# Optimization experiments

Measured on AMD Instinct MI355X. Metric: run time of the kernel, lower is better.

Reference implementation:

```python
import jax, jax.numpy as jnp
import numpy as np

BS, N, T, D, R = 64, 256, 32, 512, 8
DK = D // R  # 64 == key_feature_dim


def setup_inputs() -> dict:
    key = jax.random.key(0)
    ks = jax.random.split(key, 20)
    s = 0.02
    p = lambda k, shape: jax.random.normal(k, shape, jnp.float32) * s
    return {
        "v": jax.random.normal(ks[0], (BS, N, D), jnp.float32),
        "b": jax.random.normal(ks[1], (BS, N, D), jnp.float32),
        "v_mask": jnp.ones((BS, N), jnp.float32),
        "t": jax.random.normal(ks[2], (BS, T, D), jnp.float32),
        "t_mask": jnp.ones((BS, T), jnp.float32),
        "WG1_w": p(ks[3], (D, D)), "WG1_b": p(ks[4], (D,)),
        "WG2_w": p(ks[5], (D, D)), "WG2_b": p(ks[6], (D,)),
        "WK_w": p(ks[7], (D, D)), "WK_b": p(ks[8], (D,)),
        "WQ_w": p(ks[9], (D, D)), "WQ_b": p(ks[10], (D,)),
        "WV_w": p(ks[11], (D, D)), "WV_b": p(ks[12], (D,)),
        "tc_w": p(ks[13], (D, 1)), "tc_b": p(ks[14], (1,)),
        "tmap_w": p(ks[15], (D, N * N)), "tmap_b": p(ks[16], (N * N,)),
    }


def _forward(v, b, v_mask, t, t_mask,
             WG1_w, WG1_b, WG2_w, WG2_b, WK_w, WK_b, WQ_w, WQ_b, WV_w, WV_b,
             tc_w, tc_b, tmap_w, tmap_b):
    bs, num_obj, dim = v.shape
    n_rel = R
    dk = dim // n_rel  # dim_per_rel == dim_k

    def shape4(x):  # (bs, N, D) -> (bs, R, N, dk)
        return x.reshape(bs, num_obj, n_rel, dk).transpose(0, 2, 1, 3)

    # --- text summary branch ---
    t_m = t * t_mask[:, :, None]                       # (bs, T, D)
    tc = t_m @ tc_w + tc_b                             # (bs, T, 1)
    tc = jnp.where(t_mask[:, :, None] == 0, -jnp.inf, tc)
    t_sscore = jax.nn.sigmoid(tc)                      # sigmoid(-inf) = 0 for pad
    t_summary = jnp.einsum('btd,bt->bd', t_m, t_sscore[..., 0])   # (bs, D)
    tmap = jax.nn.relu(t_summary @ tmap_w + tmap_b)
    tmap = tmap.reshape(bs, 1, num_obj, num_obj)       # broadcast over relations

    # --- geometric pairwise score ---
    wg1 = shape4((b @ WG1_w + WG1_b) * v_mask[:, :, None])
    wg2 = shape4((b @ WG2_w + WG2_b) * v_mask[:, :, None])
    w_g = jax.nn.relu(jnp.einsum('brnd,brmd->brnm', wg1, wg2)) + tmap

    # --- scaled dot-product score ---
    wk = shape4(v @ WK_w + WK_b)
    wq = shape4(v @ WQ_w + WQ_b)
    scaled_dot = jnp.einsum('brnd,brmd->brnm', wk, wq) / jnp.sqrt(jnp.float32(dk))

    # --- combine, mask, softmax, weighted sum ---
    w_mn = jnp.log(jnp.maximum(w_g, 1e-6)) + scaled_dot
    w_mn = jnp.where((v_mask == 0)[:, None, None, :], -jnp.inf, w_mn)
    attn = jax.nn.softmax(w_mn, axis=-1)               # (bs, R, N, N)

    wv = shape4(v @ WV_w + WV_b)
    out = jnp.einsum('brnm,brmd->brnd', attn, wv)
    out = out.transpose(0, 2, 1, 3).reshape(bs, num_obj, dim)
    return out + v


def reference(v, b, v_mask, t, t_mask,
              WG1_w, WG1_b, WG2_w, WG2_b, WK_w, WK_b, WQ_w, WQ_b, WV_w, WV_b,
              tc_w, tc_b, tmap_w, tmap_b):
    return _forward(v, b, v_mask, t, t_mask,
                    WG1_w, WG1_b, WG2_w, WG2_b, WK_w, WK_b, WQ_w, WQ_b,
                    WV_w, WV_b, tc_w, tc_b, tmap_w, tmap_b)
```

## Files before the change

kernel.cpp:

```cpp
#include <hip/hip_runtime.h>
#include <math.h>

#define BS 64
#define NOBJ 256
#define TTOK 32
#define DIM 512
#define NREL 8
#define DKK 64
#define NN 65536

typedef __attribute__((ext_vector_type(8))) short bf16x8;
typedef __attribute__((ext_vector_type(4))) float f32x4;

__device__ __forceinline__ unsigned short f2bf(float x) {
    union { float f; unsigned int u; } c; c.f = x;
    unsigned int u = c.u;
    return (unsigned short)((u + 0x7fffu + ((u >> 16) & 1u)) >> 16);
}
__device__ __forceinline__ float bf2f(unsigned short h) {
    union { unsigned int u; float f; } c; c.u = ((unsigned int)h) << 16;
    return c.f;
}
__device__ __forceinline__ void gl2lds16(const unsigned short* g, unsigned short* l) {
    __builtin_amdgcn_global_load_lds((const __attribute__((address_space(1))) void*)g,
                                     (__attribute__((address_space(3))) void*)l, 16, 0, 0);
}

__global__ void k_text(const float* __restrict__ tt, const float* __restrict__ t_mask,
                       const float* __restrict__ tc_w, const float* __restrict__ tc_b,
                       unsigned short* __restrict__ ts_bf) {
    int b = blockIdx.x;
    int tid = threadIdx.x;
    __shared__ float red[TTOK][8];
    __shared__ float sc[TTOK];
    {
        int tok = tid >> 3, seg = tid & 7;
        const float* tp = tt + (size_t)(b * TTOK + tok) * DIM + seg * 64;
        const float* wp = tc_w + seg * 64;
        float s = 0.f;
#pragma unroll
        for (int i = 0; i < 16; ++i) {
            float4 a = *(const float4*)(tp + i * 4);
            float4 w = *(const float4*)(wp + i * 4);
            s += a.x * w.x + a.y * w.y + a.z * w.z + a.w * w.w;
        }
        red[tok][seg] = s;
    }
    __syncthreads();
    if (tid < TTOK) {
        float s = 0.f;
#pragma unroll
        for (int i = 0; i < 8; ++i) s += red[tid][i];
        float m = t_mask[b * TTOK + tid];
        float tc = m * s + tc_b[0];
        float sig = 1.f / (1.f + __expf(-tc));
        sc[tid] = (m != 0.f) ? m * sig : 0.f;
    }
    __syncthreads();
    for (int d = tid; d < DIM; d += 256) {
        float acc = 0.f;
#pragma unroll
        for (int tok = 0; tok < TTOK; ++tok)
            acc += tt[(size_t)(b * TTOK + tok) * DIM + d] * sc[tok];
        ts_bf[b * DIM + d] = f2bf(acc);
    }
}

__global__ void k_convert(const float* __restrict__ v, const float* __restrict__ b,
                          unsigned short* __restrict__ v_bf, unsigned short* __restrict__ b_bf) {
    const float* src = blockIdx.y ? b : v;
    unsigned short* dst = blockIdx.y ? b_bf : v_bf;
    size_t i = ((size_t)blockIdx.x * 256 + threadIdx.x) * 4;
    float4 a = *(const float4*)(src + i);
    ushort4 o;
    o.x = f2bf(a.x); o.y = f2bf(a.y); o.z = f2bf(a.z); o.w = f2bf(a.w);
    *(ushort4*)(dst + i) = o;
}

__global__ void k_wt(const float* __restrict__ w0, const float* __restrict__ w1,
                     const float* __restrict__ w2, const float* __restrict__ w3,
                     const float* __restrict__ w4, unsigned short* __restrict__ WT) {
    int wsel = blockIdx.z;
    const float* W = wsel == 0 ? w0 : wsel == 1 ? w1 : wsel == 2 ? w2 : wsel == 3 ? w3 : w4;
    int k0 = blockIdx.x * 64, d0 = blockIdx.y * 64;
    __shared__ float tile[64][65];
    int tid = threadIdx.x;
#pragma unroll
    for (int p = 0; p < 16; ++p) {
        int lin = p * 256 + tid;
        int kk = lin >> 6, dd = lin & 63;
        tile[kk][dd] = W[(size_t)(k0 + kk) * DIM + d0 + dd];
    }
    __syncthreads();
    unsigned short* outp = WT + (size_t)wsel * DIM * DIM;
#pragma unroll
    for (int p = 0; p < 16; ++p) {
        int lin = p * 256 + tid;
        int dd = lin >> 6, kk = lin & 63;
        outp[(size_t)(d0 + dd) * DIM + k0 + kk] = f2bf(tile[kk][dd]);
    }
}

__launch_bounds__(64)
__global__ void k_tmap(const unsigned short* __restrict__ ts_bf,
                       const float* __restrict__ tmap_w, const float* __restrict__ tmap_b,
                       unsigned short* __restrict__ tmap) {
    int col0 = blockIdx.x * 64;
    int lane = threadIdx.x;
    int q = lane >> 4, li = lane & 15;
    f32x4 acc[4][4];
#pragma unroll
    for (int rt = 0; rt < 4; ++rt)
#pragma unroll
        for (int ct = 0; ct < 4; ++ct) acc[rt][ct] = (f32x4){0.f, 0.f, 0.f, 0.f};

    for (int kt = 0; kt < 16; ++kt) {
        int k0 = kt * 32;
        bf16x8 a[4];
#pragma unroll
        for (int rt = 0; rt < 4; ++rt)
            a[rt] = *(const bf16x8*)(ts_bf + (size_t)(rt * 16 + li) * DIM + k0 + q * 8);
#pragma unroll
        for (int ct = 0; ct < 4; ++ct) {
            const float* wp = tmap_w + (size_t)(k0 + q * 8) * NN + col0 + ct * 16 + li;
            bf16x8 bb;
#pragma unroll
            for (int j = 0; j < 8; ++j)
                bb[j] = (short)f2bf(wp[(size_t)j * NN]);
#pragma unroll
            for (int rt = 0; rt < 4; ++rt)
                acc[rt][ct] = __builtin_amdgcn_mfma_f32_16x16x32_bf16(a[rt], bb, acc[rt][ct], 0, 0, 0);
        }
    }
#pragma unroll
    for (int ct = 0; ct < 4; ++ct) {
        int j = col0 + ct * 16 + li;
        float bias = tmap_b[j];
#pragma unroll
        for (int rt = 0; rt < 4; ++rt) {
#pragma unroll
            for (int i = 0; i < 4; ++i) {
                int bb = rt * 16 + q * 4 + i;
                float val = fmaxf(acc[rt][ct][i] + bias, 0.f);
                tmap[(size_t)bb * NN + j] = f2bf(val);
            }
        }
    }
}

__launch_bounds__(256)
__global__ void k_proj(const unsigned short* __restrict__ v_bf, const unsigned short* __restrict__ b_bf,
                       const unsigned short* __restrict__ WT,
                       const float* __restrict__ bias0, const float* __restrict__ bias1,
                       const float* __restrict__ bias2, const float* __restrict__ bias3,
                       const float* __restrict__ bias4, const float* __restrict__ v_mask,
                       unsigned short* __restrict__ wg1, unsigned short* __restrict__ wg2,
                       unsigned short* __restrict__ wk, unsigned short* __restrict__ wq,
                       unsigned short* __restrict__ wvT) {
    int bx = blockIdx.x;
    int by = blockIdx.y;
    int m0 = bx * 128;
    int wsel = by >> 2;
    const unsigned short* A = (wsel < 2) ? b_bf : v_bf;
    int tid = threadIdx.x;
    int w = tid >> 6, lane = tid & 63, q = lane >> 4, li = lane & 15;
    int rh = w & 1, ch = w >> 1;

    __shared__ __align__(16) unsigned short smem[128 * 136];
    unsigned short* As = smem;
    unsigned short* Bs = smem + 4096;

    f32x4 acc[4][4];
#pragma unroll
    for (int rt = 0; rt < 4; ++rt)
#pragma unroll
        for (int ct = 0; ct < 4; ++ct) acc[rt][ct] = (f32x4){0.f, 0.f, 0.f, 0.f};

    const unsigned short* WTb = WT + (size_t)by * 128 * DIM;

    int rho = lane >> 2;
    int qs = (lane & 3) ^ ((lane >> 3) & 3);
    int rA0 = w * 16 + rho, rA1 = (w + 4) * 16 + rho;
    const unsigned short* Ag0 = A + (size_t)(m0 + rA0) * DIM + qs * 8;
    const unsigned short* Ag1 = A + (size_t)(m0 + rA1) * DIM + qs * 8;
    const unsigned short* Bg0 = WTb + (size_t)rA0 * DIM + qs * 8;
    const unsigned short* Bg1 = WTb + (size_t)rA1 * DIM + qs * 8;
    unsigned short* Al0 = As + w * 512;
    unsigned short* Al1 = As + (w + 4) * 512;
    unsigned short* Bl0 = Bs + w * 512;
    unsigned short* Bl1 = Bs + (w + 4) * 512;

    int sseg = (q ^ ((li >> 1) & 3)) * 8;

    for (int ks = 0; ks < 16; ++ks) {
        int k0 = ks * 32;
        gl2lds16(Ag0 + k0, Al0);
        gl2lds16(Ag1 + k0, Al1);
        gl2lds16(Bg0 + k0, Bl0);
        gl2lds16(Bg1 + k0, Bl1);
        __syncthreads();
        bf16x8 af[4], bfr[4];
#pragma unroll
        for (int rt = 0; rt < 4; ++rt)
            af[rt] = *(const bf16x8*)(As + (rh * 64 + rt * 16 + li) * 32 + sseg);
#pragma unroll
        for (int ct = 0; ct < 4; ++ct)
            bfr[ct] = *(const bf16x8*)(Bs + (ch * 64 + ct * 16 + li) * 32 + sseg);
#pragma unroll
        for (int rt = 0; rt < 4; ++rt)
#pragma unroll
            for (int ct = 0; ct < 4; ++ct)
                acc[rt][ct] = __builtin_amdgcn_mfma_f32_16x16x32_bf16(af[rt], bfr[ct], acc[rt][ct], 0, 0, 0);
        __syncthreads();
    }

    const float* bias = wsel == 0 ? bias0 : wsel == 1 ? bias1 : wsel == 2 ? bias2 : wsel == 3 ? bias3 : bias4;
    int dblk = (by & 3) * 128;

    if (wsel < 4) {
#pragma unroll
        for (int ct = 0; ct < 4; ++ct) {
            int d = dblk + ch * 64 + ct * 16 + li;
            float bs = bias[d];
#pragma unroll
            for (int rt = 0; rt < 4; ++rt) {
#pragma unroll
                for (int i = 0; i < 4; ++i) {
                    int bn = m0 + rh * 64 + rt * 16 + q * 4 + i;
                    float val = acc[rt][ct][i] + bs;
                    if (wsel < 2) val *= v_mask[bn];
                    unsigned short h = f2bf(val);
                    if (wsel == 0)      wg1[(size_t)bn * DIM + d] = h;
                    else if (wsel == 1) wg2[(size_t)bn * DIM + d] = h;
                    else if (wsel == 2) wk[(size_t)bn * DIM + d] = h;
                    else                wq[(size_t)bn * DIM + d] = h;
                }
            }
        }
    } else {
        unsigned short (*T)[136] = (unsigned short (*)[136])smem;
#pragma unroll
        for (int ct = 0; ct < 4; ++ct) {
            int d_local = ch * 64 + ct * 16 + li;
            float bs = bias[dblk + d_local];
#pragma unroll
            for (int rt = 0; rt < 4; ++rt) {
#pragma unroll
                for (int i = 0; i < 4; ++i) {
                    int n_local = rh * 64 + rt * 16 + q * 4 + i;
                    T[d_local][n_local] = f2bf(acc[rt][ct][i] + bs);
                }
            }
        }
        __syncthreads();
        int b = m0 >> 8, nbase = m0 & 255;
        int dl = tid >> 1;
        int nh = (tid & 1) * 64;
        int d = dblk + dl;
        int rr = d >> 6, dk = d & 63;
        unsigned short* dst = wvT + ((size_t)(b * NREL + rr) * DKK + dk) * NOBJ + nbase + nh;
#pragma unroll
        for (int k = 0; k < 8; ++k)
            *(bf16x8*)(dst + k * 8) = *(const bf16x8*)(&T[dl][nh + k * 8]);
    }
}

__launch_bounds__(256)
__global__ void k_attn(const unsigned short* __restrict__ wg1, const unsigned short* __restrict__ wg2,
                       const unsigned short* __restrict__ wk, const unsigned short* __restrict__ wq,
                       const unsigned short* __restrict__ wvT,
                       const unsigned short* __restrict__ tmap, const float* __restrict__ v_mask,
                       const float* __restrict__ v, float* __restrict__ out) {
    int br = blockIdx.x;
    int b = br >> 3, r = br & 7;
    int tid = threadIdx.x;
    int w = tid >> 6, lane = tid & 63, q = lane >> 4, li = lane & 15;

    __shared__ __align__(16) unsigned short P_lds[4][64][36];

    bf16x8 ag[4][2], ak[4][2];
    {
        const unsigned short* g1b = wg1 + (size_t)(b * NOBJ + w * 64 + li) * DIM + r * DKK + q * 8;
        const unsigned short* kb  = wk  + (size_t)(b * NOBJ + w * 64 + li) * DIM + r * DKK + q * 8;
#pragma unroll
        for (int rt = 0; rt < 4; ++rt)
#pragma unroll
            for (int kt = 0; kt < 2; ++kt) {
                ag[rt][kt] = *(const bf16x8*)(g1b + (size_t)rt * 16 * DIM + kt * 32);
                ak[rt][kt] = *(const bf16x8*)(kb + (size_t)rt * 16 * DIM + kt * 32);
            }
    }

    f32x4 O[4][4];
    float m_[4][4], l_[4][4];
#pragma unroll
    for (int rt = 0; rt < 4; ++rt) {
#pragma unroll
        for (int dt = 0; dt < 4; ++dt) O[rt][dt] = (f32x4){0.f, 0.f, 0.f, 0.f};
#pragma unroll
        for (int i = 0; i < 4; ++i) { m_[rt][i] = -INFINITY; l_[rt][i] = 0.f; }
    }

    const unsigned short* tb = tmap + ((size_t)b << 16) + (w * 64 + q * 4) * 256 + li;

    for (int j = 0; j < 8; ++j) {
        int c0 = j * 32;
        bf16x8 bg[2][2], bq[2][2];
        {
            const unsigned short* g2b = wg2 + (size_t)(b * NOBJ + c0 + li) * DIM + r * DKK + q * 8;
            const unsigned short* qb  = wq  + (size_t)(b * NOBJ + c0 + li) * DIM + r * DKK + q * 8;
#pragma unroll
            for (int ct = 0; ct < 2; ++ct)
#pragma unroll
                for (int kt = 0; kt < 2; ++kt) {
                    bg[ct][kt] = *(const bf16x8*)(g2b + (size_t)ct * 16 * DIM + kt * 32);
                    bq[ct][kt] = *(const bf16x8*)(qb + (size_t)ct * 16 * DIM + kt * 32);
                }
        }
        float vm0 = v_mask[b * NOBJ + c0 + li];
        float vm1 = v_mask[b * NOBJ + c0 + 16 + li];

        float s[4][2][4];
#pragma unroll
        for (int rt = 0; rt < 4; ++rt) {
#pragma unroll
            for (int ct = 0; ct < 2; ++ct) {
                f32x4 aG = (f32x4){0.f, 0.f, 0.f, 0.f};
                f32x4 aK = (f32x4){0.f, 0.f, 0.f, 0.f};
#pragma unroll
                for (int kt = 0; kt < 2; ++kt) {
                    aG = __builtin_amdgcn_mfma_f32_16x16x32_bf16(ag[rt][kt], bg[ct][kt], aG, 0, 0, 0);
                    aK = __builtin_amdgcn_mfma_f32_16x16x32_bf16(ak[rt][kt], bq[ct][kt], aK, 0, 0, 0);
                }
                float vm = ct ? vm1 : vm0;
#pragma unroll
                for (int i = 0; i < 4; ++i) {
                    float tm = bf2f(tb[(rt * 16 + i) * 256 + c0 + ct * 16]);
                    float g = fmaxf(aG[i], 0.f) + tm;
                    float sv = __logf(fmaxf(g, 1e-6f)) + aK[i] * 0.125f;
                    s[rt][ct][i] = (vm == 0.f) ? -INFINITY : sv;
                }
            }
        }
#pragma unroll
        for (int rt = 0; rt < 4; ++rt) {
            float alpha[4];
#pragma unroll
            for (int i = 0; i < 4; ++i) {
                float tmax = fmaxf(s[rt][0][i], s[rt][1][i]);
                tmax = fmaxf(tmax, __shfl_xor(tmax, 1));
                tmax = fmaxf(tmax, __shfl_xor(tmax, 2));
                tmax = fmaxf(tmax, __shfl_xor(tmax, 4));
                tmax = fmaxf(tmax, __shfl_xor(tmax, 8));
                float mo = m_[rt][i];
                float mn = fmaxf(mo, tmax);
                float al = (mo == -INFINITY) ? 0.f : __expf(mo - mn);
                m_[rt][i] = mn;
                alpha[i] = al;
                float p0 = __expf(s[rt][0][i] - mn);
                float p1 = __expf(s[rt][1][i] - mn);
                float ps = p0 + p1;
                ps += __shfl_xor(ps, 1);
                ps += __shfl_xor(ps, 2);
                ps += __shfl_xor(ps, 4);
                ps += __shfl_xor(ps, 8);
                l_[rt][i] = l_[rt][i] * al + ps;
                int row = rt * 16 + q * 4 + i;
                P_lds[w][row][li] = f2bf(p0);
                P_lds[w][row][16 + li] = f2bf(p1);
            }
#pragma unroll
            for (int dt = 0; dt < 4; ++dt) {
                f32x4 o = O[rt][dt];
                o[0] *= alpha[0]; o[1] *= alpha[1]; o[2] *= alpha[2]; o[3] *= alpha[3];
                O[rt][dt] = o;
            }
        }
        bf16x8 pa[4], vb[4];
#pragma unroll
        for (int rt = 0; rt < 4; ++rt)
            pa[rt] = *(const bf16x8*)(&P_lds[w][rt * 16 + li][q * 8]);
#pragma unroll
        for (int dt = 0; dt < 4; ++dt)
            vb[dt] = *(const bf16x8*)(wvT + (size_t)(br * DKK + dt * 16 + li) * NOBJ + c0 + q * 8);
#pragma unroll
        for (int rt = 0; rt < 4; ++rt)
#pragma unroll
            for (int dt = 0; dt < 4; ++dt)
                O[rt][dt] = __builtin_amdgcn_mfma_f32_16x16x32_bf16(pa[rt], vb[dt], O[rt][dt], 0, 0, 0);
    }

#pragma unroll
    for (int rt = 0; rt < 4; ++rt) {
        float linv[4];
#pragma unroll
        for (int i = 0; i < 4; ++i) linv[i] = 1.f / l_[rt][i];
#pragma unroll
        for (int dt = 0; dt < 4; ++dt) {
#pragma unroll
            for (int i = 0; i < 4; ++i) {
                int n = w * 64 + rt * 16 + q * 4 + i;
                size_t idx = (size_t)(b * NOBJ + n) * DIM + r * DKK + dt * 16 + li;
                out[idx] = O[rt][dt][i] * linv[i] + v[idx];
            }
        }
    }
}

extern "C" void kernel_launch(void* const* d_in, const int* in_sizes, int n_in,
                              void* d_out, int out_size, void* d_ws, size_t ws_size,
                              hipStream_t stream) {
    const float* v      = (const float*)d_in[0];
    const float* b      = (const float*)d_in[1];
    const float* v_mask = (const float*)d_in[2];
    const float* t      = (const float*)d_in[3];
    const float* t_mask = (const float*)d_in[4];
    const float* WG1_w  = (const float*)d_in[5];
    const float* WG1_b  = (const float*)d_in[6];
    const float* WG2_w  = (const float*)d_in[7];
    const float* WG2_b  = (const float*)d_in[8];
    const float* WK_w   = (const float*)d_in[9];
    const float* WK_b   = (const float*)d_in[10];
    const float* WQ_w   = (const float*)d_in[11];
    const float* WQ_b   = (const float*)d_in[12];
    const float* WV_w   = (const float*)d_in[13];
    const float* WV_b   = (const float*)d_in[14];
    const float* tc_w   = (const float*)d_in[15];
    const float* tc_b   = (const float*)d_in[16];
    const float* tmap_w = (const float*)d_in[17];
    const float* tmap_b = (const float*)d_in[18];
    float* out = (float*)d_out;

    char* ws = (char*)d_ws;
    size_t off = 0;
    auto alloc = [&](size_t bytes) {
        void* p = ws + off;
        off += (bytes + 255) & ~(size_t)255;
        return p;
    };
    unsigned short* ts_bf = (unsigned short*)alloc((size_t)BS * DIM * 2);
    unsigned short* tmap  = (unsigned short*)alloc((size_t)BS * NN * 2);
    unsigned short* v_bf  = (unsigned short*)alloc((size_t)BS * NOBJ * DIM * 2);
    unsigned short* b_bf  = (unsigned short*)alloc((size_t)BS * NOBJ * DIM * 2);
    unsigned short* WT    = (unsigned short*)alloc((size_t)5 * DIM * DIM * 2);
    unsigned short* wg1   = (unsigned short*)alloc((size_t)BS * NOBJ * DIM * 2);
    unsigned short* wg2   = (unsigned short*)alloc((size_t)BS * NOBJ * DIM * 2);
    unsigned short* wk    = (unsigned short*)alloc((size_t)BS * NOBJ * DIM * 2);
    unsigned short* wq    = (unsigned short*)alloc((size_t)BS * NOBJ * DIM * 2);
    unsigned short* wvT   = (unsigned short*)alloc((size_t)BS * NOBJ * DIM * 2);

    k_text<<<dim3(BS), dim3(256), 0, stream>>>(t, t_mask, tc_w, tc_b, ts_bf);
    k_convert<<<dim3(8192, 2), dim3(256), 0, stream>>>(v, b, v_bf, b_bf);
    k_wt<<<dim3(8, 8, 5), dim3(256), 0, stream>>>(WG1_w, WG2_w, WK_w, WQ_w, WV_w, WT);
    k_tmap<<<dim3(1024), dim3(64), 0, stream>>>(ts_bf, tmap_w, tmap_b, tmap);
    k_proj<<<dim3(128, 20), dim3(256), 0, stream>>>(v_bf, b_bf, WT,
                                                    WG1_b, WG2_b, WK_b, WQ_b, WV_b, v_mask,
                                                    wg1, wg2, wk, wq, wvT);
    k_attn<<<dim3(512), dim3(256), 0, stream>>>(wg1, wg2, wk, wq, wvT, tmap, v_mask, v, out);
}
```

Before: 494.4 us.

## Stage tmap weights via LDS, deepen proj K-tile, coalesce proj stores

k_tmap moves to 256 threads that cooperatively load and convert a 32x64 weight tile into LDS with coalesced reads, replacing strided per-lane global loads. Each wave now owns 16 of the 64 batch rows. k_proj doubles the K step to 64 per LDS stage with a new XOR swizzle, halving barrier count. Its non-transposed outputs are staged through LDS and written as 16-byte vector stores instead of scattered 2-byte stores. LDS use and register pressure rise somewhat.

```diff
diff --git a/kernel.cpp b/kernel.cpp
--- a/kernel.cpp
+++ b/kernel.cpp
@@ -101,49 +101,44 @@
     }
 }
 
-__launch_bounds__(64)
+__launch_bounds__(256)
 __global__ void k_tmap(const unsigned short* __restrict__ ts_bf,
                        const float* __restrict__ tmap_w, const float* __restrict__ tmap_b,
                        unsigned short* __restrict__ tmap) {
-    int col0 = blockIdx.x * 64;
-    int lane = threadIdx.x;
-    int q = lane >> 4, li = lane & 15;
-    f32x4 acc[4][4];
-#pragma unroll
-    for (int rt = 0; rt < 4; ++rt)
-#pragma unroll
-        for (int ct = 0; ct < 4; ++ct) acc[rt][ct] = (f32x4){0.f, 0.f, 0.f, 0.f};
-
-    for (int kt = 0; kt < 16; ++kt) {
-        int k0 = kt * 32;
-        bf16x8 a[4];
-#pragma unroll
-        for (int rt = 0; rt < 4; ++rt)
-            a[rt] = *(const bf16x8*)(ts_bf + (size_t)(rt * 16 + li) * DIM + k0 + q * 8);
+    int j0 = blockIdx.x * 64;
+    int tid = threadIdx.x;
+    int w = tid >> 6, lane = tid & 63, q = lane >> 4, li = lane & 15;
+    __shared__ __align__(16) unsigned short Bt[64][40];
+    f32x4 acc[4];
+#pragma unroll
+    for (int ct = 0; ct < 4; ++ct) acc[ct] = (f32x4){0.f, 0.f, 0.f, 0.f};
+
+    for (int ks = 0; ks < 16; ++ks) {
+        int k0 = ks * 32;
+#pragma unroll
+        for (int p = 0; p < 8; ++p) {
+            int kk = (tid >> 6) + p * 4;
+            int c = tid & 63;
+            Bt[c][kk] = f2bf(tmap_w[(size_t)(k0 + kk) * NN + j0 + c]);
+        }
+        __syncthreads();
+        bf16x8 a = *(const bf16x8*)(ts_bf + (size_t)(w * 16 + li) * DIM + k0 + q * 8);
 #pragma unroll
         for (int ct = 0; ct < 4; ++ct) {
-            const float* wp = tmap_w + (size_t)(k0 + q * 8) * NN + col0 + ct * 16 + li;
-            bf16x8 bb;
-#pragma unroll
-            for (int j = 0; j < 8; ++j)
-                bb[j] = (short)f2bf(wp[(size_t)j * NN]);
-#pragma unroll
-            for (int rt = 0; rt < 4; ++rt)
-                acc[rt][ct] = __builtin_amdgcn_mfma_f32_16x16x32_bf16(a[rt], bb, acc[rt][ct], 0, 0, 0);
-        }
+            bf16x8 bb = *(const bf16x8*)(&Bt[ct * 16 + li][q * 8]);
+            acc[ct] = __builtin_amdgcn_mfma_f32_16x16x32_bf16(a, bb, acc[ct], 0, 0, 0);
+        }
+        __syncthreads();
     }
 #pragma unroll
     for (int ct = 0; ct < 4; ++ct) {
-        int j = col0 + ct * 16 + li;
+        int j = j0 + ct * 16 + li;
         float bias = tmap_b[j];
 #pragma unroll
-        for (int rt = 0; rt < 4; ++rt) {
-#pragma unroll
-            for (int i = 0; i < 4; ++i) {
-                int bb = rt * 16 + q * 4 + i;
-                float val = fmaxf(acc[rt][ct][i] + bias, 0.f);
-                tmap[(size_t)bb * NN + j] = f2bf(val);
-            }
+        for (int i = 0; i < 4; ++i) {
+            int bb = w * 16 + q * 4 + i;
+            float val = fmaxf(acc[ct][i] + bias, 0.f);
+            tmap[(size_t)bb * NN + j] = f2bf(val);
         }
     }
 }
@@ -168,7 +163,7 @@
 
     __shared__ __align__(16) unsigned short smem[128 * 136];
     unsigned short* As = smem;
-    unsigned short* Bs = smem + 4096;
+    unsigned short* Bs = smem + 8192;
 
     f32x4 acc[4][4];
 #pragma unroll
@@ -178,45 +173,58 @@
 
     const unsigned short* WTb = WT + (size_t)by * 128 * DIM;
 
-    int rho = lane >> 2;
-    int qs = (lane & 3) ^ ((lane >> 3) & 3);
-    int rA0 = w * 16 + rho, rA1 = (w + 4) * 16 + rho;
-    const unsigned short* Ag0 = A + (size_t)(m0 + rA0) * DIM + qs * 8;
-    const unsigned short* Ag1 = A + (size_t)(m0 + rA1) * DIM + qs * 8;
-    const unsigned short* Bg0 = WTb + (size_t)rA0 * DIM + qs * 8;
-    const unsigned short* Bg1 = WTb + (size_t)rA1 * DIM + qs * 8;
-    unsigned short* Al0 = As + w * 512;
-    unsigned short* Al1 = As + (w + 4) * 512;
-    unsigned short* Bl0 = Bs + w * 512;
-    unsigned short* Bl1 = Bs + (w + 4) * 512;
-
-    int sseg = (q ^ ((li >> 1) & 3)) * 8;
-
-    for (int ks = 0; ks < 16; ++ks) {
-        int k0 = ks * 32;
-        gl2lds16(Ag0 + k0, Al0);
-        gl2lds16(Ag1 + k0, Al1);
-        gl2lds16(Bg0 + k0, Bl0);
-        gl2lds16(Bg1 + k0, Bl1);
-        __syncthreads();
-        bf16x8 af[4], bfr[4];
-#pragma unroll
-        for (int rt = 0; rt < 4; ++rt)
-            af[rt] = *(const bf16x8*)(As + (rh * 64 + rt * 16 + li) * 32 + sseg);
-#pragma unroll
-        for (int ct = 0; ct < 4; ++ct)
-            bfr[ct] = *(const bf16x8*)(Bs + (ch * 64 + ct * 16 + li) * 32 + sseg);
-#pragma unroll
-        for (int rt = 0; rt < 4; ++rt)
+    int rl = lane >> 3;
+    int lseg = (lane & 7) ^ rl;
+    const unsigned short* Agp[4];
+    const unsigned short* Bgp[4];
+    unsigned short* Alp[4];
+    unsigned short* Blp[4];
+#pragma unroll
+    for (int c4 = 0; c4 < 4; ++c4) {
+        int c = w * 4 + c4;
+        int row = c * 8 + rl;
+        Agp[c4] = A + (size_t)(m0 + row) * DIM + lseg * 8;
+        Bgp[c4] = WTb + (size_t)row * DIM + lseg * 8;
+        Alp[c4] = As + c * 512;
+        Blp[c4] = Bs + c * 512;
+    }
+
+    int arow = (rh * 64 + li) * 64;
+    int brow = (ch * 64 + li) * 64;
+    int sseg0 = ((q) ^ (li & 7)) * 8;
+    int sseg1 = ((4 + q) ^ (li & 7)) * 8;
+
+    for (int ks = 0; ks < 8; ++ks) {
+        int k0 = ks * 64;
+#pragma unroll
+        for (int c4 = 0; c4 < 4; ++c4) {
+            gl2lds16(Agp[c4] + k0, Alp[c4]);
+            gl2lds16(Bgp[c4] + k0, Blp[c4]);
+        }
+        __syncthreads();
+#pragma unroll
+        for (int j = 0; j < 2; ++j) {
+            int sseg = j ? sseg1 : sseg0;
+            bf16x8 af[4], bfr[4];
+#pragma unroll
+            for (int rt = 0; rt < 4; ++rt)
+                af[rt] = *(const bf16x8*)(As + arow + rt * 1024 + sseg);
 #pragma unroll
             for (int ct = 0; ct < 4; ++ct)
-                acc[rt][ct] = __builtin_amdgcn_mfma_f32_16x16x32_bf16(af[rt], bfr[ct], acc[rt][ct], 0, 0, 0);
+                bfr[ct] = *(const bf16x8*)(Bs + brow + ct * 1024 + sseg);
+#pragma unroll
+            for (int rt = 0; rt < 4; ++rt)
+#pragma unroll
+                for (int ct = 0; ct < 4; ++ct)
+                    acc[rt][ct] = __builtin_amdgcn_mfma_f32_16x16x32_bf16(af[rt], bfr[ct], acc[rt][ct], 0, 0, 0);
+        }
         __syncthreads();
     }
 
     const float* bias = wsel == 0 ? bias0 : wsel == 1 ? bias1 : wsel == 2 ? bias2 : wsel == 3 ? bias3 : bias4;
     int dblk = (by & 3) * 128;
 
+    unsigned short (*T)[136] = (unsigned short (*)[136])smem;
     if (wsel < 4) {
 #pragma unroll
         for (int ct = 0; ct < 4; ++ct) {
@@ -226,42 +234,47 @@
             for (int rt = 0; rt < 4; ++rt) {
 #pragma unroll
                 for (int i = 0; i < 4; ++i) {
-                    int bn = m0 + rh * 64 + rt * 16 + q * 4 + i;
+                    int nl = rh * 64 + rt * 16 + q * 4 + i;
                     float val = acc[rt][ct][i] + bs;
-                    if (wsel < 2) val *= v_mask[bn];
-                    unsigned short h = f2bf(val);
-                    if (wsel == 0)      wg1[(size_t)bn * DIM + d] = h;
-                    else if (wsel == 1) wg2[(size_t)bn * DIM + d] = h;
-                    else if (wsel == 2) wk[(size_t)bn * DIM + d] = h;
-                    else                wq[(size_t)bn * DIM + d] = h;
+                    if (wsel < 2) val *= v_mask[m0 + nl];
+                    T[nl][ch * 64 + ct * 16 + li] = f2bf(val);
                 }
             }
         }
+        __syncthreads();
+        unsigned short* dstb = wsel == 0 ? wg1 : wsel == 1 ? wg2 : wsel == 2 ? wk : wq;
+        int dc = lane & 15;
+#pragma unroll
+        for (int rr = 0; rr < 8; ++rr) {
+            int outer = w * 32 + rr * 4 + (lane >> 4);
+            *(bf16x8*)(dstb + (size_t)(m0 + outer) * DIM + dblk + dc * 8) =
+                *(const bf16x8*)(&T[outer][dc * 8]);
+        }
     } else {
-        unsigned short (*T)[136] = (unsigned short (*)[136])smem;
 #pragma unroll
         for (int ct = 0; ct < 4; ++ct) {
-            int d_local = ch * 64 + ct * 16 + li;
-            float bs = bias[dblk + d_local];
+            int dl = ch * 64 + ct * 16 + li;
+            float bs = bias[dblk + dl];
 #pragma unroll
             for (int rt = 0; rt < 4; ++rt) {
 #pragma unroll
                 for (int i = 0; i < 4; ++i) {
-                    int n_local = rh * 64 + rt * 16 + q * 4 + i;
-                    T[d_local][n_local] = f2bf(acc[rt][ct][i] + bs);
+                    int nl = rh * 64 + rt * 16 + q * 4 + i;
+                    T[dl][nl] = f2bf(acc[rt][ct][i] + bs);
                 }
             }
         }
         __syncthreads();
         int b = m0 >> 8, nbase = m0 & 255;
-        int dl = tid >> 1;
-        int nh = (tid & 1) * 64;
-        int d = dblk + dl;
-        int rr = d >> 6, dk = d & 63;
-        unsigned short* dst = wvT + ((size_t)(b * NREL + rr) * DKK + dk) * NOBJ + nbase + nh;
-#pragma unroll
-        for (int k = 0; k < 8; ++k)
-            *(bf16x8*)(dst + k * 8) = *(const bf16x8*)(&T[dl][nh + k * 8]);
+        int dc = lane & 15;
+#pragma unroll
+        for (int rr = 0; rr < 8; ++rr) {
+            int outer = w * 32 + rr * 4 + (lane >> 4);
+            int d = dblk + outer;
+            int r = d >> 6, dk = d & 63;
+            *(bf16x8*)(wvT + ((size_t)(b * NREL + r) * DKK + dk) * NOBJ + nbase + dc * 8) =
+                *(const bf16x8*)(&T[outer][dc * 8]);
+        }
     }
 }
 
@@ -452,7 +465,7 @@
     k_text<<<dim3(BS), dim3(256), 0, stream>>>(t, t_mask, tc_w, tc_b, ts_bf);
     k_convert<<<dim3(8192, 2), dim3(256), 0, stream>>>(v, b, v_bf, b_bf);
     k_wt<<<dim3(8, 8, 5), dim3(256), 0, stream>>>(WG1_w, WG2_w, WK_w, WQ_w, WV_w, WT);
-    k_tmap<<<dim3(1024), dim3(64), 0, stream>>>(ts_bf, tmap_w, tmap_b, tmap);
+    k_tmap<<<dim3(1024), dim3(256), 0, stream>>>(ts_bf, tmap_w, tmap_b, tmap);
     k_proj<<<dim3(128, 20), dim3(256), 0, stream>>>(v_bf, b_bf, WT,
                                                     WG1_b, WG2_b, WK_b, WQ_b, WV_b, v_mask,
                                                     wg1, wg2, wk, wq, wvT);
```

Measured after the change: 471.1 us. 1.05x faster.
